# Performance work log

Hardware: AMD Instinct MI355X
Metric: run time of the kernel (lower is better)

The kernel has to match this reference:

```python
import jax, jax.numpy as jnp
import numpy as np

D = 1024
H = 16
HD = D // H
FF = 4 * D
EPS = 1e-6


def layernorm(x, g, b):
    mu = jnp.mean(x, axis=-1, keepdims=True)
    var = jnp.mean((x - mu) ** 2, axis=-1, keepdims=True)
    return (x - mu) * jax.lax.rsqrt(var + EPS) * g + b


def setup_inputs() -> dict:
    key = jax.random.key(0)
    ks = jax.random.split(key, 12)
    s = 0.02
    return {
        "x": jax.random.normal(ks[0], (8, 1024, D), dtype=jnp.float32),
        "qkv_w": jax.random.normal(ks[1], (3 * D, D), dtype=jnp.float32) * s,
        "qkv_b": jnp.zeros((3 * D,), dtype=jnp.float32),
        "proj_w": jax.random.normal(ks[2], (D, D), dtype=jnp.float32) * s,
        "proj_b": jnp.zeros((D,), dtype=jnp.float32),
        "fc1_w": jax.random.normal(ks[3], (FF, D), dtype=jnp.float32) * s,
        "fc1_b": jnp.zeros((FF,), dtype=jnp.float32),
        "fc2_w": jax.random.normal(ks[4], (D, FF), dtype=jnp.float32) * s,
        "fc2_b": jnp.zeros((D,), dtype=jnp.float32),
        "ln1_g": jnp.ones((D,), dtype=jnp.float32),
        "ln1_b": jnp.zeros((D,), dtype=jnp.float32),
        "ln2_g": jnp.ones((D,), dtype=jnp.float32),
        "ln2_b": jnp.zeros((D,), dtype=jnp.float32),
    }


def reference(x, qkv_w, qkv_b, proj_w, proj_b, fc1_w, fc1_b, fc2_w, fc2_b,
              ln1_g, ln1_b, ln2_g, ln2_b):
    B, S, _ = x.shape
    # attention branch
    h = layernorm(x, ln1_g, ln1_b)
    qkv = h @ qkv_w.T + qkv_b                      # [B,S,3D]
    qkv = qkv.reshape(B, S, 3, H, HD)
    q, k, v = qkv[:, :, 0], qkv[:, :, 1], qkv[:, :, 2]  # [B,S,H,HD]
    scores = jnp.einsum('bshd,bthd->bhst', q, k) * (HD ** -0.5)
    attn = jax.nn.softmax(scores, axis=-1)
    ctx = jnp.einsum('bhst,bthd->bshd', attn, v).reshape(B, S, D)
    x = x + ctx @ proj_w.T + proj_b
    # mlp branch
    h = layernorm(x, ln2_g, ln2_b)
    h = jax.nn.gelu(h @ fc1_w.T + fc1_b, approximate=False)
    x = x + h @ fc2_w.T + fc2_b
    return x
```

## Files before the change

kernel.cpp:

```cpp
#include <hip/hip_runtime.h>
#include <stdint.h>

typedef unsigned short u16;
typedef __attribute__((ext_vector_type(8))) short bf16x8;
typedef __attribute__((ext_vector_type(4))) float f32x4;

__device__ __forceinline__ u16 f2bf(float f) {
    union { float f; uint32_t u; } v; v.f = f;
    uint32_t r = (v.u + 0x7FFFu + ((v.u >> 16) & 1u)) >> 16;
    return (u16)r;
}

__device__ __forceinline__ void g2l16(const u16* g, u16* l) {
    __builtin_amdgcn_global_load_lds(
        (const __attribute__((address_space(1))) uint32_t*)g,
        (__attribute__((address_space(3))) uint32_t*)l, 16, 0, 0);
}

__device__ __forceinline__ float gelu_f(float x) {
    float x2 = x * x;
    float u = x * (0.7978845608028654f + 0.035677408136300125f * x2);
    float t = exp2f(-2.8853900817779268f * fabsf(u));
    float th = (1.0f - t) / (1.0f + t);
    th = (u < 0.0f) ? -th : th;
    return 0.5f * x * (1.0f + th);
}

__global__ __launch_bounds__(256) void cvt_kernel(const float* __restrict__ in,
                                                  u16* __restrict__ out, int n4) {
    int i = blockIdx.x * 256 + threadIdx.x;
    if (i < n4) {
        float4 v = ((const float4*)in)[i];
        uint2 o;
        o.x = (uint32_t)f2bf(v.x) | ((uint32_t)f2bf(v.y) << 16);
        o.y = (uint32_t)f2bf(v.z) | ((uint32_t)f2bf(v.w) << 16);
        ((uint2*)out)[i] = o;
    }
}

__global__ __launch_bounds__(256) void ln_kernel(const float* __restrict__ x,
                                                 const float* __restrict__ g,
                                                 const float* __restrict__ beta,
                                                 u16* __restrict__ out) {
    int row = blockIdx.x;
    int tid = threadIdx.x;
    const float4 v = ((const float4*)(x + (size_t)row * 1024))[tid];
    float s  = v.x + v.y + v.z + v.w;
    float sq = v.x*v.x + v.y*v.y + v.z*v.z + v.w*v.w;
    #pragma unroll
    for (int off = 32; off; off >>= 1) {
        s  += __shfl_xor(s,  off, 64);
        sq += __shfl_xor(sq, off, 64);
    }
    __shared__ float rs[4], rq[4];
    int w = tid >> 6;
    if ((tid & 63) == 0) { rs[w] = s; rq[w] = sq; }
    __syncthreads();
    s  = rs[0] + rs[1] + rs[2] + rs[3];
    sq = rq[0] + rq[1] + rq[2] + rq[3];
    float mu   = s * (1.0f / 1024.0f);
    float var  = sq * (1.0f / 1024.0f) - mu * mu;
    float rstd = rsqrtf(var + 1e-6f);
    float4 gv = ((const float4*)g)[tid];
    float4 bv = ((const float4*)beta)[tid];
    uint2 o;
    o.x = (uint32_t)f2bf((v.x - mu) * rstd * gv.x + bv.x) |
          ((uint32_t)f2bf((v.y - mu) * rstd * gv.y + bv.y) << 16);
    o.y = (uint32_t)f2bf((v.z - mu) * rstd * gv.z + bv.z) |
          ((uint32_t)f2bf((v.w - mu) * rstd * gv.w + bv.w) << 16);
    ((uint2*)(out + (size_t)row * 1024))[tid] = o;
}

template<int ACT, int RES, int OUTMODE>
__global__ __launch_bounds__(512) void gemm2_kernel(
    const u16* __restrict__ A, const u16* __restrict__ W,
    const float* __restrict__ bias, const float* __restrict__ res,
    void* __restrict__ Cout, u16* __restrict__ vtb, int M, int N, int K)
{
    const int BM = 128, BN = 256, BK = 64;
    __shared__ u16 sA[2 * BM * BK];
    __shared__ u16 sB[2 * BN * BK];

    int tid = threadIdx.x;
    int lane = tid & 63, wid = tid >> 6;
    int wm = wid >> 2, wn = wid & 3;
    int q = lane & 15, g = lane >> 4;

    int MT = M >> 7;
    int nwg = gridDim.x;
    int chunk = nwg >> 3;
    int bid = blockIdx.x;
    int wg = (bid & 7) * chunk + (bid >> 3);
    int mt = wg % MT, nt = wg / MT;
    int m0 = mt << 7, n0 = nt << 8;
    const int NT = K >> 6;

    const u16* srcA[2]; const u16* srcB[4];
    u16* dstA[2]; u16* dstB[4];
    #pragma unroll
    for (int l = 0; l < 2; l++) {
        int idx = l * 512 + tid, row = idx >> 3;
        int col = ((idx & 7) * 8) ^ ((row & 7) << 3);
        srcA[l] = A + (size_t)(m0 + row) * K + col;
        dstA[l] = sA + (l * 512 + wid * 64) * 8;
    }
    #pragma unroll
    for (int l = 0; l < 4; l++) {
        int idx = l * 512 + tid, row = idx >> 3;
        int col = ((idx & 7) * 8) ^ ((row & 7) << 3);
        srcB[l] = W + (size_t)(n0 + row) * K + col;
        dstB[l] = sB + (l * 512 + wid * 64) * 8;
    }

    #define STAGE(bf, t) { int ko = (t) * 64; int boA = (bf) * (BM * BK); int boB = (bf) * (BN * BK); \
        g2l16(srcA[0] + ko, dstA[0] + boA); g2l16(srcA[1] + ko, dstA[1] + boA); \
        g2l16(srcB[0] + ko, dstB[0] + boB); g2l16(srcB[1] + ko, dstB[1] + boB); \
        g2l16(srcB[2] + ko, dstB[2] + boB); g2l16(srcB[3] + ko, dstB[3] + boB); }

    f32x4 acc[4][4] = {};

    STAGE(0, 0);
    STAGE(1, 1);
    asm volatile("s_waitcnt vmcnt(6)\n" ::: "memory");
    __builtin_amdgcn_s_barrier();

    int buf = 0;
    for (int t = 0; t < NT; t++) {
        const u16* bA = sA + buf * (BM * BK);
        const u16* bB = sB + buf * (BN * BK);
        bf16x8 af[2][4], bfr[2][4];
        #pragma unroll
        for (int ks = 0; ks < 2; ks++) {
            #pragma unroll
            for (int i = 0; i < 4; i++) {
                int rowL = wm * 64 + i * 16 + q;
                int colE = (ks * 32 + g * 8) ^ ((rowL & 7) << 3);
                af[ks][i] = *(const bf16x8*)(bA + rowL * 64 + colE);
            }
            #pragma unroll
            for (int j = 0; j < 4; j++) {
                int rowL = wn * 64 + j * 16 + q;
                int colE = (ks * 32 + g * 8) ^ ((rowL & 7) << 3);
                bfr[ks][j] = *(const bf16x8*)(bB + rowL * 64 + colE);
            }
        }
        asm volatile("s_waitcnt lgkmcnt(0)\n" ::: "memory");
        __builtin_amdgcn_s_barrier();
        bool pre = (t + 2 < NT);
        if (pre) STAGE(buf, t + 2);
        #pragma unroll
        for (int ks = 0; ks < 2; ks++)
            #pragma unroll
            for (int i = 0; i < 4; i++)
                #pragma unroll
                for (int j = 0; j < 4; j++)
                    acc[i][j] = __builtin_amdgcn_mfma_f32_16x16x32_bf16(af[ks][i], bfr[ks][j], acc[i][j], 0, 0, 0);
        if (pre) { asm volatile("s_waitcnt vmcnt(6)\n" ::: "memory"); }
        else     { asm volatile("s_waitcnt vmcnt(0)\n" ::: "memory"); }
        __builtin_amdgcn_s_barrier();
        buf ^= 1;
    }
    #undef STAGE

    #pragma unroll
    for (int i = 0; i < 4; i++) {
        #pragma unroll
        for (int j = 0; j < 4; j++) {
            int col = n0 + wn * 64 + j * 16 + q;
            float bz = bias[col];
            int row0 = m0 + wm * 64 + i * 16 + g * 4;
            float vv[4];
            #pragma unroll
            for (int r = 0; r < 4; r++) {
                float v = acc[i][j][r] + bz;
                if (ACT == 1) v = gelu_f(v);
                if (RES) v += res[(size_t)(row0 + r) * N + col];
                vv[r] = v;
            }
            if (OUTMODE == 0) {
                #pragma unroll
                for (int r = 0; r < 4; r++) ((float*)Cout)[(size_t)(row0 + r) * N + col] = vv[r];
            } else if (OUTMODE == 1) {
                #pragma unroll
                for (int r = 0; r < 4; r++) ((u16*)Cout)[(size_t)(row0 + r) * N + col] = f2bf(vv[r]);
            } else {
                if (col < 2048) {
                    #pragma unroll
                    for (int r = 0; r < 4; r++) ((u16*)Cout)[(size_t)(row0 + r) * 2048 + col] = f2bf(vv[r]);
                } else {
                    int hd = col & 63, hh = (col >> 6) - 32;
                    int b_ = row0 >> 10, s_ = row0 & 1023;
                    ushort4 pk = { f2bf(vv[0]), f2bf(vv[1]), f2bf(vv[2]), f2bf(vv[3]) };
                    *(ushort4*)(vtb + (((size_t)(b_ * 16 + hh) * 64 + hd) << 10) + s_) = pk;
                }
            }
        }
    }
}

__global__ __launch_bounds__(256) void attn_kernel(const u16* __restrict__ qk,
                                                   const u16* __restrict__ vt,
                                                   u16* __restrict__ ctx) {
    int bid = blockIdx.x;
    int qt = bid & 15;
    int h  = (bid >> 4) & 15;
    int b  = bid >> 8;
    int tid = threadIdx.x, lane = tid & 63, w = tid >> 6;
    int q = lane & 15, g = lane >> 4;

    __shared__ u16 sK[2][64 * 72];
    __shared__ u16 sV[2][64 * 72];

    const size_t tokBase = (size_t)b * 1024 * 2048 + (size_t)h * 64;
    const u16* vbase = vt + (size_t)(b * 16 + h) * 64 * 1024;
    const float SC = 0.125f * 1.44269504088896f;

    const u16* qrow = qk + tokBase + (size_t)(qt * 64 + w * 16 + q) * 2048;
    bf16x8 qf0 = *(const bf16x8*)(qrow + g * 8);
    bf16x8 qf1 = *(const bf16x8*)(qrow + 32 + g * 8);

    int r0 = tid >> 3, c0 = (tid & 7) * 8;
    int kp0 = 8 * ((r0 >> 2) & 3) + 4 * ((r0 >> 4) & 1) + (r0 & 3);
    int kp1 = 32 + kp0;

    {
        uint4 k0 = *(const uint4*)(qk + tokBase + (size_t)kp0 * 2048 + 1024 + c0);
        uint4 k1 = *(const uint4*)(qk + tokBase + (size_t)kp1 * 2048 + 1024 + c0);
        uint4 v0 = *(const uint4*)(vbase + (size_t)r0 * 1024 + c0);
        uint4 v1 = *(const uint4*)(vbase + (size_t)(32 + r0) * 1024 + c0);
        *(uint4*)(&sK[0][r0 * 72 + c0]) = k0;
        *(uint4*)(&sK[0][(32 + r0) * 72 + c0]) = k1;
        *(uint4*)(&sV[0][r0 * 72 + c0]) = v0;
        *(uint4*)(&sV[0][(32 + r0) * 72 + c0]) = v1;
    }
    __syncthreads();

    float m_run = -1e30f, l_run = 0.0f;
    f32x4 o[4];
    #pragma unroll
    for (int n = 0; n < 4; n++) o[n] = (f32x4){0.f, 0.f, 0.f, 0.f};

    for (int kt = 0; kt < 16; kt++) {
        int cur = kt & 1;
        uint4 kn0 = {}, kn1 = {}, vn0 = {}, vn1 = {};
        if (kt < 15) {
            size_t kb = tokBase + (size_t)((kt + 1) * 64) * 2048 + 1024 + c0;
            kn0 = *(const uint4*)(qk + kb + (size_t)kp0 * 2048);
            kn1 = *(const uint4*)(qk + kb + (size_t)kp1 * 2048);
            vn0 = *(const uint4*)(vbase + (size_t)r0 * 1024 + (kt + 1) * 64 + c0);
            vn1 = *(const uint4*)(vbase + (size_t)(32 + r0) * 1024 + (kt + 1) * 64 + c0);
        }

        f32x4 s[4];
        #pragma unroll
        for (int c = 0; c < 4; c++) {
            s[c] = (f32x4){0.f, 0.f, 0.f, 0.f};
            bf16x8 a0 = *(const bf16x8*)(&sK[cur][(c * 16 + q) * 72 + g * 8]);
            bf16x8 a1 = *(const bf16x8*)(&sK[cur][(c * 16 + q) * 72 + 32 + g * 8]);
            s[c] = __builtin_amdgcn_mfma_f32_16x16x32_bf16(a0, qf0, s[c], 0, 0, 0);
            s[c] = __builtin_amdgcn_mfma_f32_16x16x32_bf16(a1, qf1, s[c], 0, 0, 0);
        }
        float ps[16];
        #pragma unroll
        for (int c = 0; c < 4; c++)
            #pragma unroll
            for (int r = 0; r < 4; r++) ps[c * 4 + r] = s[c][r] * SC;

        float tm = ps[0];
        #pragma unroll
        for (int i = 1; i < 16; i++) tm = fmaxf(tm, ps[i]);
        tm = fmaxf(tm, __shfl_xor(tm, 16, 64));
        tm = fmaxf(tm, __shfl_xor(tm, 32, 64));

        if (!__all(tm - m_run <= 8.0f)) {
            float nm = fmaxf(m_run, tm);
            float f = exp2f(m_run - nm);
            float fr[4];
            #pragma unroll
            for (int r = 0; r < 4; r++) fr[r] = __shfl(f, g * 4 + r, 64);
            #pragma unroll
            for (int n = 0; n < 4; n++)
                #pragma unroll
                for (int r = 0; r < 4; r++) o[n][r] *= fr[r];
            l_run *= f;
            m_run = nm;
        }

        float ts = 0.0f;
        #pragma unroll
        for (int i = 0; i < 16; i++) { ps[i] = exp2f(ps[i] - m_run); ts += ps[i]; }
        ts += __shfl_xor(ts, 16, 64);
        ts += __shfl_xor(ts, 32, 64);
        l_run += ts;

        bf16x8 pf0, pf1;
        #pragma unroll
        for (int j = 0; j < 4; j++) {
            pf0[j]     = (short)f2bf(ps[j]);
            pf0[4 + j] = (short)f2bf(ps[4 + j]);
            pf1[j]     = (short)f2bf(ps[8 + j]);
            pf1[4 + j] = (short)f2bf(ps[12 + j]);
        }

        if (kt < 15) {
            *(uint4*)(&sK[cur ^ 1][r0 * 72 + c0]) = kn0;
            *(uint4*)(&sK[cur ^ 1][(32 + r0) * 72 + c0]) = kn1;
            *(uint4*)(&sV[cur ^ 1][r0 * 72 + c0]) = vn0;
            *(uint4*)(&sV[cur ^ 1][(32 + r0) * 72 + c0]) = vn1;
        }

        #pragma unroll
        for (int n = 0; n < 4; n++) {
            bf16x8 v0 = *(const bf16x8*)(&sV[cur][(n * 16 + q) * 72 + g * 8]);
            o[n] = __builtin_amdgcn_mfma_f32_16x16x32_bf16(pf0, v0, o[n], 0, 0, 0);
        }
        #pragma unroll
        for (int n = 0; n < 4; n++) {
            bf16x8 v1 = *(const bf16x8*)(&sV[cur][(n * 16 + q) * 72 + 32 + g * 8]);
            o[n] = __builtin_amdgcn_mfma_f32_16x16x32_bf16(pf1, v1, o[n], 0, 0, 0);
        }
        __syncthreads();
    }

    float inv = 1.0f / l_run;
    float ir[4];
    #pragma unroll
    for (int r = 0; r < 4; r++) ir[r] = __shfl(inv, g * 4 + r, 64);
    size_t outBase = ((size_t)b * 1024 + qt * 64 + w * 16) * 1024 + (size_t)h * 64;
    #pragma unroll
    for (int n = 0; n < 4; n++)
        #pragma unroll
        for (int r = 0; r < 4; r++)
            ctx[outBase + (size_t)(g * 4 + r) * 1024 + n * 16 + q] = f2bf(o[n][r] * ir[r]);
}

extern "C" void kernel_launch(void* const* d_in, const int* in_sizes, int n_in,
                              void* d_out, int out_size, void* d_ws, size_t ws_size,
                              hipStream_t stream) {
    const float* x      = (const float*)d_in[0];
    const float* qkv_w  = (const float*)d_in[1];
    const float* qkv_b  = (const float*)d_in[2];
    const float* proj_w = (const float*)d_in[3];
    const float* proj_b = (const float*)d_in[4];
    const float* fc1_w  = (const float*)d_in[5];
    const float* fc1_b  = (const float*)d_in[6];
    const float* fc2_w  = (const float*)d_in[7];
    const float* fc2_b  = (const float*)d_in[8];
    const float* ln1_g  = (const float*)d_in[9];
    const float* ln1_b  = (const float*)d_in[10];
    const float* ln2_g  = (const float*)d_in[11];
    const float* ln2_b  = (const float*)d_in[12];
    float* out = (float*)d_out;

    char* ws = (char*)d_ws;
    u16* wq = (u16*)(ws);
    u16* wp = (u16*)(ws + 6291456);
    u16* w1 = (u16*)(ws + 8388608);
    u16* w2 = (u16*)(ws + 16777216);
    char* pool = ws + 25165824;
    u16* hbuf = (u16*)(pool);
    u16* qkb  = (u16*)(pool + 16777216);
    u16* vtb  = (u16*)(pool + 50331648);
    u16* ctxb = (u16*)(pool);
    u16* h2b  = (u16*)(pool + 16777216);
    u16* a1b  = (u16*)(pool + 33554432);

    cvt_kernel<<<3072, 256, 0, stream>>>(qkv_w, wq, 786432);
    cvt_kernel<<<1024, 256, 0, stream>>>(proj_w, wp, 262144);
    cvt_kernel<<<4096, 256, 0, stream>>>(fc1_w, w1, 1048576);
    cvt_kernel<<<4096, 256, 0, stream>>>(fc2_w, w2, 1048576);

    ln_kernel<<<8192, 256, 0, stream>>>(x, ln1_g, ln1_b, hbuf);
    gemm2_kernel<0,0,2><<<768, 512, 0, stream>>>(hbuf, wq, qkv_b, nullptr, qkb, vtb, 8192, 3072, 1024);
    attn_kernel<<<2048, 256, 0, stream>>>(qkb, vtb, ctxb);
    gemm2_kernel<0,1,0><<<256, 512, 0, stream>>>(ctxb, wp, proj_b, x, out, nullptr, 8192, 1024, 1024);
    ln_kernel<<<8192, 256, 0, stream>>>(out, ln2_g, ln2_b, h2b);
    gemm2_kernel<1,0,1><<<1024, 512, 0, stream>>>(h2b, w1, fc1_b, nullptr, a1b, nullptr, 8192, 4096, 1024);
    gemm2_kernel<0,1,0><<<256, 512, 0, stream>>>(a1b, w2, fc2_b, out, out, nullptr, 8192, 1024, 4096);
}
```

Before: 530.0 us.

## Add 256x256-tile GEMM with interleaved staged loads for QKV and FC1

Adds a new GEMM kernel with 256x256 output tiles and 8 waves, each owning a 128x64 sub-tile. Its inner loop is split into quarter-steps that interleave LDS reads, async global-to-LDS prefetch and MFMA blocks, with s_setprio raising priority around the MFMAs. The QKV and FC1 projections switch to it, which halves their grid sizes and raises operand reuse per loaded byte. The attention kernel also gets a block-index swizzle across XCDs and setprio around its MFMAs. The trade-offs are heavier LDS use (128KB+), more registers for the accumulators, and many barriers inside the loop.

Result: no change. 534.8 us (+0.9%).

```diff
diff --git a/kernel.cpp b/kernel.cpp
--- a/kernel.cpp
+++ b/kernel.cpp
@@ -72,103 +72,125 @@
 }
 
 template<int ACT, int RES, int OUTMODE>
-__global__ __launch_bounds__(512) void gemm2_kernel(
+__global__ __launch_bounds__(512, 2) void gemm8_kernel(
     const u16* __restrict__ A, const u16* __restrict__ W,
     const float* __restrict__ bias, const float* __restrict__ res,
     void* __restrict__ Cout, u16* __restrict__ vtb, int M, int N, int K)
 {
-    const int BM = 128, BN = 256, BK = 64;
-    __shared__ u16 sA[2 * BM * BK];
-    __shared__ u16 sB[2 * BN * BK];
+    __shared__ u16 sA[2][256 * 64];
+    __shared__ u16 sB[2][256 * 64];
+    __shared__ u16 sDump[4096];
 
     int tid = threadIdx.x;
     int lane = tid & 63, wid = tid >> 6;
     int wm = wid >> 2, wn = wid & 3;
     int q = lane & 15, g = lane >> 4;
 
-    int MT = M >> 7;
-    int nwg = gridDim.x;
+    int MT = M >> 8;
+    int nwg = gridDim.x, bid = blockIdx.x;
     int chunk = nwg >> 3;
-    int bid = blockIdx.x;
     int wg = (bid & 7) * chunk + (bid >> 3);
     int mt = wg % MT, nt = wg / MT;
-    int m0 = mt << 7, n0 = nt << 8;
-    const int NT = K >> 6;
-
-    const u16* srcA[2]; const u16* srcB[4];
-    u16* dstA[2]; u16* dstB[4];
-    #pragma unroll
-    for (int l = 0; l < 2; l++) {
-        int idx = l * 512 + tid, row = idx >> 3;
-        int col = ((idx & 7) * 8) ^ ((row & 7) << 3);
-        srcA[l] = A + (size_t)(m0 + row) * K + col;
-        dstA[l] = sA + (l * 512 + wid * 64) * 8;
-    }
-    #pragma unroll
-    for (int l = 0; l < 4; l++) {
-        int idx = l * 512 + tid, row = idx >> 3;
-        int col = ((idx & 7) * 8) ^ ((row & 7) << 3);
-        srcB[l] = W + (size_t)(n0 + row) * K + col;
-        dstB[l] = sB + (l * 512 + wid * 64) * 8;
-    }
-
-    #define STAGE(bf, t) { int ko = (t) * 64; int boA = (bf) * (BM * BK); int boB = (bf) * (BN * BK); \
-        g2l16(srcA[0] + ko, dstA[0] + boA); g2l16(srcA[1] + ko, dstA[1] + boA); \
-        g2l16(srcB[0] + ko, dstB[0] + boB); g2l16(srcB[1] + ko, dstB[1] + boB); \
-        g2l16(srcB[2] + ko, dstB[2] + boB); g2l16(srcB[3] + ko, dstB[3] + boB); }
-
-    f32x4 acc[4][4] = {};
-
-    STAGE(0, 0);
-    STAGE(1, 1);
-    asm volatile("s_waitcnt vmcnt(6)\n" ::: "memory");
-    __builtin_amdgcn_s_barrier();
-
-    int buf = 0;
-    for (int t = 0; t < NT; t++) {
-        const u16* bA = sA + buf * (BM * BK);
-        const u16* bB = sB + buf * (BN * BK);
-        bf16x8 af[2][4], bfr[2][4];
-        #pragma unroll
-        for (int ks = 0; ks < 2; ks++) {
-            #pragma unroll
-            for (int i = 0; i < 4; i++) {
-                int rowL = wm * 64 + i * 16 + q;
-                int colE = (ks * 32 + g * 8) ^ ((rowL & 7) << 3);
-                af[ks][i] = *(const bf16x8*)(bA + rowL * 64 + colE);
-            }
-            #pragma unroll
-            for (int j = 0; j < 4; j++) {
-                int rowL = wn * 64 + j * 16 + q;
-                int colE = (ks * 32 + g * 8) ^ ((rowL & 7) << 3);
-                bfr[ks][j] = *(const bf16x8*)(bB + rowL * 64 + colE);
-            }
-        }
-        asm volatile("s_waitcnt lgkmcnt(0)\n" ::: "memory");
-        __builtin_amdgcn_s_barrier();
-        bool pre = (t + 2 < NT);
-        if (pre) STAGE(buf, t + 2);
-        #pragma unroll
-        for (int ks = 0; ks < 2; ks++)
-            #pragma unroll
-            for (int i = 0; i < 4; i++)
-                #pragma unroll
-                for (int j = 0; j < 4; j++)
-                    acc[i][j] = __builtin_amdgcn_mfma_f32_16x16x32_bf16(af[ks][i], bfr[ks][j], acc[i][j], 0, 0, 0);
-        if (pre) { asm volatile("s_waitcnt vmcnt(6)\n" ::: "memory"); }
-        else     { asm volatile("s_waitcnt vmcnt(0)\n" ::: "memory"); }
-        __builtin_amdgcn_s_barrier();
-        buf ^= 1;
-    }
-    #undef STAGE
-
-    #pragma unroll
-    for (int i = 0; i < 4; i++) {
+    int m0 = mt << 8, n0 = nt << 8;
+    int NT = K >> 6, NU = NT >> 1;
+
+    int srow = lane >> 3;
+    int scol = (lane & 7) * 8;
+    const u16* Ab = A + (size_t)m0 * K;
+    const u16* Wb = W + (size_t)n0 * K;
+
+    auto stA = [&](int par, int tile, int rs, bool ok) {
+        int c = scol ^ (srow << 3);
+        g2l16(ok ? (Ab + (size_t)(rs + srow) * K + (tile << 6) + c) : (Ab + c),
+              ok ? (&sA[par][rs << 6]) : sDump);
+    };
+    auto stB = [&](int par, int tile, int rs, bool ok) {
+        int c = scol ^ (srow << 3);
+        g2l16(ok ? (Wb + (size_t)(rs + srow) * K + (tile << 6) + c) : (Wb + c),
+              ok ? (&sB[par][rs << 6]) : sDump);
+    };
+    auto stAQ = [&](int par, int tile, int qq, bool ok) {
+        stA(par, tile, qq * 64 + wid * 8, ok);
+        stA(par, tile, 128 + qq * 64 + wid * 8, ok);
+    };
+    auto stBN = [&](int par, int tile, int nh, bool ok) {
+        int rs = (wid >> 2) * 64 + (wid & 3) * 8 + nh * 32;
+        stB(par, tile, rs, ok);
+        stB(par, tile, rs + 128, ok);
+    };
+
+    f32x4 acc[8][4] = {};
+    bf16x8 af[2][4], bv[2][2];
+
+#define RD_A(par, mh) { _Pragma("unroll") for (int i = 0; i < 4; i++) { \
+    int rowL = wm * 128 + (mh) * 64 + i * 16 + q; \
+    _Pragma("unroll") for (int ks = 0; ks < 2; ks++) { \
+        int colE = (ks * 32 + g * 8) ^ ((rowL & 7) << 3); \
+        af[ks][i] = *(const bf16x8*)(&sA[par][rowL * 64 + colE]); } } }
+#define RD_B(par, nh) { _Pragma("unroll") for (int j = 0; j < 2; j++) { \
+    int rowL = wn * 64 + (nh) * 32 + j * 16 + q; \
+    _Pragma("unroll") for (int ks = 0; ks < 2; ks++) { \
+        int colE = (ks * 32 + g * 8) ^ ((rowL & 7) << 3); \
+        bv[ks][j] = *(const bf16x8*)(&sB[par][rowL * 64 + colE]); } } }
+#define MFMA16(mh, nh) { \
+    __builtin_amdgcn_s_barrier(); \
+    asm volatile("s_waitcnt lgkmcnt(0)" ::: "memory"); \
+    __builtin_amdgcn_sched_barrier(0); \
+    __builtin_amdgcn_s_setprio(1); \
+    _Pragma("unroll") for (int ks = 0; ks < 2; ks++) \
+    _Pragma("unroll") for (int i = 0; i < 4; i++) \
+    _Pragma("unroll") for (int j = 0; j < 2; j++) \
+        acc[(mh)*4+i][(nh)*2+j] = __builtin_amdgcn_mfma_f32_16x16x32_bf16( \
+            af[ks][i], bv[ks][j], acc[(mh)*4+i][(nh)*2+j], 0, 0, 0); \
+    __builtin_amdgcn_s_setprio(0); }
+#define VM4 asm volatile("s_waitcnt vmcnt(4)" ::: "memory")
+#define BAR __builtin_amdgcn_s_barrier()
+
+    stAQ(0, 0, 0, true); stBN(0, 0, 0, true);
+    stAQ(0, 0, 1, true); stBN(0, 0, 1, true);
+    stAQ(1, 1, 0, true); stBN(1, 1, 0, true);
+    VM4; BAR;
+
+    for (int u = 0; u < NU; u++) {
+        int t = 2 * u;
+        bool ok2 = (t + 2 < NT), ok3 = (t + 3 < NT);
+        RD_A(0, 0); RD_B(0, 0);
+        stAQ(1, t + 1, 1, true); stBN(1, t + 1, 1, true);
+        MFMA16(0, 0); BAR;
+        RD_B(0, 1);
+        MFMA16(0, 1); BAR;
+        RD_A(0, 1); RD_B(0, 0);
+        stAQ(0, t + 2, 0, ok2);
+        MFMA16(1, 0); BAR;
+        RD_B(0, 1);
+        stBN(0, t + 2, 0, ok2);
+        MFMA16(1, 1); VM4; BAR;
+        RD_A(1, 0); RD_B(1, 0);
+        stAQ(0, t + 2, 1, ok2); stBN(0, t + 2, 1, ok2);
+        MFMA16(0, 0); BAR;
+        RD_B(1, 1);
+        MFMA16(0, 1); BAR;
+        RD_A(1, 1); RD_B(1, 0);
+        stAQ(1, t + 3, 0, ok3);
+        MFMA16(1, 0); BAR;
+        RD_B(1, 1);
+        stBN(1, t + 3, 0, ok3);
+        MFMA16(1, 1); VM4; BAR;
+    }
+    asm volatile("s_waitcnt vmcnt(0)" ::: "memory");
+#undef RD_A
+#undef RD_B
+#undef MFMA16
+#undef VM4
+#undef BAR
+
+    #pragma unroll
+    for (int i = 0; i < 8; i++) {
         #pragma unroll
         for (int j = 0; j < 4; j++) {
             int col = n0 + wn * 64 + j * 16 + q;
             float bz = bias[col];
-            int row0 = m0 + wm * 64 + i * 16 + g * 4;
+            int row0 = m0 + wm * 128 + i * 16 + g * 4;
             float vv[4];
             #pragma unroll
             for (int r = 0; r < 4; r++) {
@@ -198,13 +220,131 @@
     }
 }
 
+template<int ACT, int RES, int OUTMODE>
+__global__ __launch_bounds__(512) void gemm2_kernel(
+    const u16* __restrict__ A, const u16* __restrict__ W,
+    const float* __restrict__ bias, const float* __restrict__ res,
+    void* __restrict__ Cout, u16* __restrict__ vtb, int M, int N, int K)
+{
+    const int BM = 128, BN = 256, BK = 64;
+    __shared__ u16 sA[2 * BM * BK];
+    __shared__ u16 sB[2 * BN * BK];
+
+    int tid = threadIdx.x;
+    int lane = tid & 63, wid = tid >> 6;
+    int wm = wid >> 2, wn = wid & 3;
+    int q = lane & 15, g = lane >> 4;
+
+    int MT = M >> 7;
+    int nwg = gridDim.x;
+    int chunk = nwg >> 3;
+    int bid = blockIdx.x;
+    int wg = (bid & 7) * chunk + (bid >> 3);
+    int mt = wg % MT, nt = wg / MT;
+    int m0 = mt << 7, n0 = nt << 8;
+    const int NT = K >> 6;
+
+    const u16* srcA[2]; const u16* srcB[4];
+    u16* dstA[2]; u16* dstB[4];
+    #pragma unroll
+    for (int l = 0; l < 2; l++) {
+        int idx = l * 512 + tid, row = idx >> 3;
+        int col = ((idx & 7) * 8) ^ ((row & 7) << 3);
+        srcA[l] = A + (size_t)(m0 + row) * K + col;
+        dstA[l] = sA + (l * 512 + wid * 64) * 8;
+    }
+    #pragma unroll
+    for (int l = 0; l < 4; l++) {
+        int idx = l * 512 + tid, row = idx >> 3;
+        int col = ((idx & 7) * 8) ^ ((row & 7) << 3);
+        srcB[l] = W + (size_t)(n0 + row) * K + col;
+        dstB[l] = sB + (l * 512 + wid * 64) * 8;
+    }
+
+    #define STAGE(bf, t) { int ko = (t) * 64; int boA = (bf) * (BM * BK); int boB = (bf) * (BN * BK); \
+        g2l16(srcA[0] + ko, dstA[0] + boA); g2l16(srcA[1] + ko, dstA[1] + boA); \
+        g2l16(srcB[0] + ko, dstB[0] + boB); g2l16(srcB[1] + ko, dstB[1] + boB); \
+        g2l16(srcB[2] + ko, dstB[2] + boB); g2l16(srcB[3] + ko, dstB[3] + boB); }
+
+    f32x4 acc[4][4] = {};
+
+    STAGE(0, 0);
+    STAGE(1, 1);
+    asm volatile("s_waitcnt vmcnt(6)\n" ::: "memory");
+    __builtin_amdgcn_s_barrier();
+
+    int buf = 0;
+    for (int t = 0; t < NT; t++) {
+        const u16* bA = sA + buf * (BM * BK);
+        const u16* bB = sB + buf * (BN * BK);
+        bf16x8 af[2][4], bfr[2][4];
+        #pragma unroll
+        for (int ks = 0; ks < 2; ks++) {
+            #pragma unroll
+            for (int i = 0; i < 4; i++) {
+                int rowL = wm * 64 + i * 16 + q;
+                int colE = (ks * 32 + g * 8) ^ ((rowL & 7) << 3);
+                af[ks][i] = *(const bf16x8*)(bA + rowL * 64 + colE);
+            }
+            #pragma unroll
+            for (int j = 0; j < 4; j++) {
+                int rowL = wn * 64 + j * 16 + q;
+                int colE = (ks * 32 + g * 8) ^ ((rowL & 7) << 3);
+                bfr[ks][j] = *(const bf16x8*)(bB + rowL * 64 + colE);
+            }
+        }
+        asm volatile("s_waitcnt lgkmcnt(0)\n" ::: "memory");
+        __builtin_amdgcn_s_barrier();
+        bool pre = (t + 2 < NT);
+        if (pre) STAGE(buf, t + 2);
+        #pragma unroll
+        for (int ks = 0; ks < 2; ks++)
+            #pragma unroll
+            for (int i = 0; i < 4; i++)
+                #pragma unroll
+                for (int j = 0; j < 4; j++)
+                    acc[i][j] = __builtin_amdgcn_mfma_f32_16x16x32_bf16(af[ks][i], bfr[ks][j], acc[i][j], 0, 0, 0);
+        if (pre) { asm volatile("s_waitcnt vmcnt(6)\n" ::: "memory"); }
+        else     { asm volatile("s_waitcnt vmcnt(0)\n" ::: "memory"); }
+        __builtin_amdgcn_s_barrier();
+        buf ^= 1;
+    }
+    #undef STAGE
+
+    #pragma unroll
+    for (int i = 0; i < 4; i++) {
+        #pragma unroll
+        for (int j = 0; j < 4; j++) {
+            int col = n0 + wn * 64 + j * 16 + q;
+            float bz = bias[col];
+            int row0 = m0 + wm * 64 + i * 16 + g * 4;
+            float vv[4];
+            #pragma unroll
+            for (int r = 0; r < 4; r++) {
+                float v = acc[i][j][r] + bz;
+                if (ACT == 1) v = gelu_f(v);
+                if (RES) v += res[(size_t)(row0 + r) * N + col];
+                vv[r] = v;
+            }
+            if (OUTMODE == 0) {
+                #pragma unroll
+                for (int r = 0; r < 4; r++) ((float*)Cout)[(size_t)(row0 + r) * N + col] = vv[r];
+            } else {
+                #pragma unroll
+                for (int r = 0; r < 4; r++) ((u16*)Cout)[(size_t)(row0 + r) * N + col] = f2bf(vv[r]);
+            }
+        }
+    }
+}
+
 __global__ __launch_bounds__(256) void attn_kernel(const u16* __restrict__ qk,
                                                    const u16* __restrict__ vt,
                                                    u16* __restrict__ ctx) {
     int bid = blockIdx.x;
-    int qt = bid & 15;
-    int h  = (bid >> 4) & 15;
-    int b  = bid >> 8;
+    int idx = (bid & 7) * 256 + (bid >> 3);
+    int qt = idx & 15;
+    int h  = (idx >> 4) & 15;
+    int b  = idx >> 8;
     int tid = threadIdx.x, lane = tid & 63, w = tid >> 6;
     int q = lane & 15, g = lane >> 4;
 
@@ -252,6 +392,7 @@
         }
 
         f32x4 s[4];
+        __builtin_amdgcn_s_setprio(1);
         #pragma unroll
         for (int c = 0; c < 4; c++) {
             s[c] = (f32x4){0.f, 0.f, 0.f, 0.f};
@@ -260,6 +401,7 @@
             s[c] = __builtin_amdgcn_mfma_f32_16x16x32_bf16(a0, qf0, s[c], 0, 0, 0);
             s[c] = __builtin_amdgcn_mfma_f32_16x16x32_bf16(a1, qf1, s[c], 0, 0, 0);
         }
+        __builtin_amdgcn_s_setprio(0);
         float ps[16];
         #pragma unroll
         for (int c = 0; c < 4; c++)
@@ -309,6 +451,7 @@
             *(uint4*)(&sV[cur ^ 1][(32 + r0) * 72 + c0]) = vn1;
         }
 
+        __builtin_amdgcn_s_setprio(1);
         #pragma unroll
         for (int n = 0; n < 4; n++) {
             bf16x8 v0 = *(const bf16x8*)(&sV[cur][(n * 16 + q) * 72 + g * 8]);
@@ -319,6 +462,7 @@
             bf16x8 v1 = *(const bf16x8*)(&sV[cur][(n * 16 + q) * 72 + 32 + g * 8]);
             o[n] = __builtin_amdgcn_mfma_f32_16x16x32_bf16(pf1, v1, o[n], 0, 0, 0);
         }
+        __builtin_amdgcn_s_setprio(0);
         __syncthreads();
     }
 
@@ -371,10 +515,10 @@
     cvt_kernel<<<4096, 256, 0, stream>>>(fc2_w, w2, 1048576);
 
     ln_kernel<<<8192, 256, 0, stream>>>(x, ln1_g, ln1_b, hbuf);
-    gemm2_kernel<0,0,2><<<768, 512, 0, stream>>>(hbuf, wq, qkv_b, nullptr, qkb, vtb, 8192, 3072, 1024);
+    gemm8_kernel<0,0,2><<<384, 512, 0, stream>>>(hbuf, wq, qkv_b, nullptr, qkb, vtb, 8192, 3072, 1024);
     attn_kernel<<<2048, 256, 0, stream>>>(qkb, vtb, ctxb);
     gemm2_kernel<0,1,0><<<256, 512, 0, stream>>>(ctxb, wp, proj_b, x, out, nullptr, 8192, 1024, 1024);
     ln_kernel<<<8192, 256, 0, stream>>>(out, ln2_g, ln2_b, h2b);
-    gemm2_kernel<1,0,1><<<1024, 512, 0, stream>>>(h2b, w1, fc1_b, nullptr, a1b, nullptr, 8192, 4096, 1024);
+    gemm8_kernel<1,0,1><<<512, 512, 0, stream>>>(h2b, w1, fc1_b, nullptr, a1b, nullptr, 8192, 4096, 1024);
     gemm2_kernel<0,1,0><<<256, 512, 0, stream>>>(a1b, w2, fc2_b, out, out, nullptr, 8192, 1024, 4096);
 }
```
